# Kernel optimization log

Measured on AMD Instinct MI355X. Metric: run time of the kernel, lower is better.

The kernel has to match this reference:

```python
import jax, jax.numpy as jnp
import numpy as np

B, T, C, H, U = 16, 2048, 512, 4, 250
L, R = 1, 1              # l_order, r_order -> depthwise kernel size 3
K = L + R + 1
SMOOTH, NOISE = 1.0, 0.0  # smooth_factor, noise_threshold


def setup_inputs() -> dict:
    key = jax.random.key(0)
    k0, k1, k2, k3 = jax.random.split(key, 4)
    hidden = jax.random.normal(k0, (B, T, C), dtype=jnp.float32)
    mask = jnp.ones((B, 1, T), dtype=jnp.float32)
    target_label_length = jax.random.randint(k1, (B,), 0, U).astype(jnp.int32)
    # parameters
    conv_w = jax.random.normal(k2, (C, 1, K), dtype=jnp.float32) / np.sqrt(K)   # depthwise Conv1d weight [O, I/g=1, K]
    conv_b = jnp.zeros((C,), dtype=jnp.float32)
    lin_w = jax.random.normal(k3, (1, C), dtype=jnp.float32) / np.sqrt(C)       # cif_output Linear(idim, 1)
    lin_b = jnp.zeros((1,), dtype=jnp.float32)
    sigma = jnp.full((H,), 0.5, dtype=jnp.float32)
    sigma_bias = jnp.zeros((H,), dtype=jnp.float32)
    return {
        "hidden": hidden, "mask": mask, "target_label_length": target_label_length,
        "max_token": U, "conv_w": conv_w, "conv_b": conv_b,
        "lin_w": lin_w, "lin_b": lin_b, "sigma": sigma, "sigma_bias": sigma_bias,
    }


def reference(hidden, mask, target_label_length, max_token, conv_w, conv_b, lin_w, lin_b, sigma, sigma_bias):
    b, t, c = hidden.shape
    h = sigma.shape[0]
    # --- alpha prediction branch ---
    context = jnp.swapaxes(hidden, 1, 2)                       # [B, C, T]
    queries = jnp.pad(context, ((0, 0), (0, 0), (L, R)))       # ConstantPad1d((l, r), 0)
    memory = jax.lax.conv_general_dilated(
        queries, conv_w, window_strides=(1,), padding='VALID',
        feature_group_count=c, dimension_numbers=('NCH', 'OIH', 'NCH'))
    memory = memory + conv_b[None, :, None]
    out = jnp.swapaxes(memory + context, 1, 2)                 # [B, T, C]  (dropout = identity in eval)
    out = jax.nn.relu(out)
    out = out @ lin_w.T + lin_b                                # [B, T, 1]
    alphas = jax.nn.relu(jax.nn.sigmoid(out) * SMOOTH - NOISE)
    mask_bt1 = jnp.swapaxes(mask, -1, -2)                      # [B, T, 1]
    alphas = (alphas * mask_bt1)[..., 0]                       # [B, T]
    mask_bt = mask_bt1[..., 0]                                 # [B, T]
    # --- CIF scaling to target length ---
    target_length = target_label_length.astype(jnp.float32)   # [B]
    token_num = alphas.sum(-1)                                 # [B] (pre-scaling, as in torch)
    alphas = alphas * (target_length / token_num)[:, None]
    alignment = jnp.cumsum(alphas, axis=-1)                    # [B, T]
    # --- Gaussian soft-segment attention ---
    fire_positions = jnp.arange(max_token, dtype=alphas.dtype) + 0.5            # [U]
    dist = fire_positions[None, None, :, None] - alignment[:, None, None, :]    # [B, 1, U, T]
    scores = -(dist * sigma[None, :, None, None]) ** 2 + sigma_bias[None, :, None, None]  # [B, H, U, T]
    scores = jnp.where(mask_bt[:, None, None, :] > 0, scores, -jnp.inf)
    weights = jax.nn.softmax(scores, axis=-1)                  # [B, H, U, T]
    n_hidden = hidden.reshape(b, t, h, c // h).transpose(0, 2, 1, 3)            # [B, H, T, Dh]
    acoustic = jnp.einsum('bhut,bhtd->bhud', weights, n_hidden)                 # [B, H, U, Dh]
    acoustic_embeds = acoustic.transpose(0, 2, 1, 3).reshape(b, max_token, c)   # [B, U, C]
    return acoustic_embeds, token_num, alphas
```

## Files before the change

kernel.cpp:

```cpp
#include <hip/hip_runtime.h>
#include <hip/hip_bf16.h>

namespace {
constexpr int kB = 16, kT = 2048, kC = 512, kH = 4, kU = 250, kDH = 128;
constexpr int kDS = 4;
constexpr int kDW = 32;
constexpr int kTT = 256;
constexpr int kNST = kT / kTT;
constexpr int kPitch = 264;
}

typedef __attribute__((ext_vector_type(8))) short short8;
typedef __attribute__((ext_vector_type(4))) float float4v;

__device__ __forceinline__ short f2bf(float x) {
    union { float f; unsigned int u; } v; v.f = x;
    unsigned int r = (v.u + 0x7FFFu + ((v.u >> 16) & 1u)) >> 16;
    return (short)r;
}

__global__ __launch_bounds__(256) void k1_alpha(
    const float* __restrict__ hid, const float* __restrict__ mask,
    const float* __restrict__ conv_w, const float* __restrict__ conv_b,
    const float* __restrict__ lin_w, const float* __restrict__ lin_b,
    float* __restrict__ alpha_raw)
{
    __shared__ float halo[4][2][512];
    const int wave = threadIdx.x >> 6, lane = threadIdx.x & 63;
    const int b = blockIdx.x >> 6;
    const int tblk = (blockIdx.x & 63) << 5;
    const int t0 = tblk + wave * 8;
    const int c0 = lane * 8;

    float cw[24], cb[8], lw[8];
    #pragma unroll
    for (int i = 0; i < 6; i++) *(float4*)&cw[i*4] = ((const float4*)(conv_w + c0*3))[i];
    *(float4*)&cb[0] = *(const float4*)(conv_b + c0);
    *(float4*)&cb[4] = *(const float4*)(conv_b + c0 + 4);
    *(float4*)&lw[0] = *(const float4*)(lin_w + c0);
    *(float4*)&lw[4] = *(const float4*)(lin_w + c0 + 4);
    const float lb = lin_b[0];

    float r[10][8];
    const float* base = hid + ((size_t)b * kT + t0) * kC + c0;
    #pragma unroll
    for (int i = 1; i <= 8; i++) {
        const float* p = base + (ptrdiff_t)(i - 1) * kC;
        *(float4*)&r[i][0] = *(const float4*)p;
        *(float4*)&r[i][4] = *(const float4*)(p + 4);
    }
    *(float4*)&halo[wave][0][c0]     = *(float4*)&r[1][0];
    *(float4*)&halo[wave][0][c0 + 4] = *(float4*)&r[1][4];
    *(float4*)&halo[wave][1][c0]     = *(float4*)&r[8][0];
    *(float4*)&halo[wave][1][c0 + 4] = *(float4*)&r[8][4];

    if (wave == 0) {
        if (tblk > 0) {
            const float* p = base - kC;
            *(float4*)&r[0][0] = *(const float4*)p;
            *(float4*)&r[0][4] = *(const float4*)(p + 4);
        } else {
            #pragma unroll
            for (int j = 0; j < 8; j++) r[0][j] = 0.f;
        }
    }
    if (wave == 3) {
        if (tblk + 32 < kT) {
            const float* p = base + 8 * kC;
            *(float4*)&r[9][0] = *(const float4*)p;
            *(float4*)&r[9][4] = *(const float4*)(p + 4);
        } else {
            #pragma unroll
            for (int j = 0; j < 8; j++) r[9][j] = 0.f;
        }
    }
    __syncthreads();
    if (wave > 0) {
        *(float4*)&r[0][0] = *(float4*)&halo[wave - 1][1][c0];
        *(float4*)&r[0][4] = *(float4*)&halo[wave - 1][1][c0 + 4];
    }
    if (wave < 3) {
        *(float4*)&r[9][0] = *(float4*)&halo[wave + 1][0][c0];
        *(float4*)&r[9][4] = *(float4*)&halo[wave + 1][0][c0 + 4];
    }

    float sums[8];
    #pragma unroll
    for (int j = 0; j < 8; j++) {
        float acc = 0.f;
        #pragma unroll
        for (int k = 0; k < 8; k++) {
            float m = fmaf(r[j][k], cw[k*3],
                      fmaf(r[j+1][k], cw[k*3+1],
                      fmaf(r[j+2][k], cw[k*3+2], cb[k])));
            float v = m + r[j+1][k];
            v = v > 0.f ? v : 0.f;
            acc = fmaf(v, lw[k], acc);
        }
        #pragma unroll
        for (int off = 32; off >= 1; off >>= 1) acc += __shfl_xor(acc, off, 64);
        sums[j] = acc;
    }
    if (lane == 0) {
        #pragma unroll
        for (int j = 0; j < 8; j++) {
            float s = sums[j] + lb;
            float a = 1.f / (1.f + expf(-s));
            alpha_raw[(size_t)b * kT + t0 + j] = a * mask[(size_t)b * kT + t0 + j];
        }
    }
}

__global__ __launch_bounds__(1024) void k3_attn(
    const float* __restrict__ hid, const float* __restrict__ alpha_raw,
    const float* __restrict__ mask, const int* __restrict__ target,
    const float* __restrict__ sigma,
    float* __restrict__ out_ac, float* __restrict__ out_tok, float* __restrict__ out_alpha)
{
    __shared__ float al_s[kT];
    __shared__ unsigned short bT[2][kDW * kPitch];
    __shared__ float woff[16];
    __shared__ float s_tot;

    const int ds = blockIdx.x, h = blockIdx.y, b = blockIdx.z;
    const int tid = threadIdx.x;
    const int wave = tid >> 6, lane = tid & 63;
    const int lm = lane & 15, quad = lane >> 4;
    const float sig = sigma[h];

    const int dl = tid & 7;
    const int p  = tid >> 3;
    const float* hrow = hid + (size_t)b * kT * kC + h * kDH + ds * kDW + dl * 4;

    float4 a0, a1;
    {
        const float* src = hrow + (size_t)(2 * p) * kC;
        a0 = *(const float4*)src;
        a1 = *(const float4*)(src + kC);
    }

    float2 av = ((const float2*)(alpha_raw + (size_t)b * kT))[tid];
    float2 mv = ((const float2*)(mask + (size_t)b * kT))[tid];
    const float p0 = av.x, p1 = av.x + av.y;
    const float s = p1;
    float sc = s;
    #pragma unroll
    for (int off = 1; off <= 32; off <<= 1) {
        float v = __shfl_up(sc, off, 64);
        sc = (lane >= off) ? sc + v : sc;
    }
    if (lane == 63) woff[wave] = sc;
    __syncthreads();
    if (tid == 0) {
        float run = 0.f;
        #pragma unroll
        for (int w = 0; w < 16; w++) { float x = woff[w]; woff[w] = run; run += x; }
        s_tot = run;
    }
    __syncthreads();
    const float tot = s_tot;
    const float scale = (tot != 0.f) ? ((float)target[b] / tot) : 0.f;
    const float basev = woff[wave] + (sc - s);
    {
        float c0 = (basev + p0) * scale;
        float c1 = (basev + p1) * scale;
        float2 alv;
        alv.x = (mv.x > 0.f) ? c0 : 1.0e30f;
        alv.y = (mv.y > 0.f) ? c1 : 1.0e30f;
        ((float2*)al_s)[tid] = alv;
    }
    if (ds == 0 && h == 0) {
        if (tid == 0) out_tok[b] = tot;
        float2 oa; oa.x = av.x * scale; oa.y = av.y * scale;
        ((float2*)(out_alpha + (size_t)b * kT))[tid] = oa;
    }
    __syncthreads();

    const int u_base = wave * 16;
    const float du = (float)(u_base + lm) + 0.5f;
    const float dusig = du * sig;
    int pos = 0;
    #pragma unroll
    for (int stp = 1024; stp >= 1; stp >>= 1) {
        int np = pos + stp;
        pos = (al_s[np - 1] < du) ? np : pos;
    }
    float d1 = (pos < kT) ? al_s[pos] - du : 3.0e30f;
    float d0 = (pos > 0) ? du - al_s[pos - 1] : 3.0e30f;
    float dmin = fminf(d0, d1);
    float ms = fminf(dmin, 1.0e4f) * sig;
    const float mu_pos = ms * ms;

    float dmax_l = fminf(dmin, 1.0e4f);
    #pragma unroll
    for (int off = 8; off >= 1; off >>= 1) dmax_l = fmaxf(dmax_l, __shfl_xor(dmax_l, off, 64));
    const float c21 = (sig > 1e-3f) ? 21.0f / (sig * sig) : 9.0e60f;
    const float bound = sqrtf(fmaf(dmax_l, dmax_l, c21));
    const float lo_b = (float)u_base + 0.5f - bound;
    const float hi_b = (float)u_base + 15.5f + bound;
    int p_lo = 0, p_hi = 0;
    #pragma unroll
    for (int stp = 1024; stp >= 1; stp >>= 1) {
        int n1 = p_lo + stp; p_lo = (al_s[n1 - 1] < lo_b) ? n1 : p_lo;
        int n2 = p_hi + stp; p_hi = (al_s[n2 - 1] < hi_b) ? n2 : p_hi;
    }
    const int ks_lo = p_lo >> 5;
    const int ks_end = (p_hi + 31) >> 5;

    float4v acc0 = (float4v)(0.f), acc1 = (float4v)(0.f);
    float lsum = 0.f;

    int buf = 0;
    for (int st = 0; st < kNST; st++) {
        {
            const float* q0 = (const float*)&a0;
            const float* q1 = (const float*)&a1;
            #pragma unroll
            for (int e = 0; e < 4; e++) {
                unsigned int lo = (unsigned int)(unsigned short)f2bf(q0[e]);
                unsigned int hi = (unsigned int)(unsigned short)f2bf(q1[e]);
                *(unsigned int*)&bT[buf][(dl * 4 + e) * kPitch + 2 * p] = lo | (hi << 16);
            }
        }
        __syncthreads();
        if (st + 1 < kNST) {
            const float* src = hrow + (size_t)((st + 1) * kTT + 2 * p) * kC;
            a0 = *(const float4*)src;
            a1 = *(const float4*)(src + kC);
        }

        #pragma unroll
        for (int ks = 0; ks < 8; ks++) {
            const int kg = st * 8 + ks;
            if (kg < ks_lo || kg >= ks_end) continue;
            const int kb = kg * 32;

            float alv[8];
            *(float4*)&alv[0] = *(const float4*)&al_s[kb + quad * 8];
            *(float4*)&alv[4] = *(const float4*)&al_s[kb + quad * 8 + 4];

            short8 afrag;
            #pragma unroll
            for (int j = 0; j < 8; j++) {
                float d = fmaf(-alv[j], sig, dusig);
                float e = __expf(fmaf(-d, d, mu_pos));
                lsum += e;
                afrag[j] = f2bf(e);
            }
            short8 bf0 = *(const short8*)&bT[buf][lm * kPitch + ks * 32 + quad * 8];
            short8 bf1 = *(const short8*)&bT[buf][(16 + lm) * kPitch + ks * 32 + quad * 8];
            acc0 = __builtin_amdgcn_mfma_f32_16x16x32_bf16(afrag, bf0, acc0, 0, 0, 0);
            acc1 = __builtin_amdgcn_mfma_f32_16x16x32_bf16(afrag, bf1, acc1, 0, 0, 0);
        }
        buf ^= 1;
    }

    float lv = lsum;
    lv += __shfl_xor(lv, 16, 64);
    lv += __shfl_xor(lv, 32, 64);
    #pragma unroll
    for (int r = 0; r < 4; r++) {
        const int ur = quad * 4 + r;
        float rl = __shfl(lv, ur, 64);
        float linv = (rl > 1e-30f) ? 1.f / rl : 0.f;
        const int u = u_base + ur;
        if (u < kU) {
            float* dst = out_ac + ((size_t)(b * kU + u)) * kC + h * kDH + ds * kDW + lm;
            dst[0]  = acc0[r] * linv;
            dst[16] = acc1[r] * linv;
        }
    }
}

extern "C" void kernel_launch(void* const* d_in, const int* in_sizes, int n_in,
                              void* d_out, int out_size, void* d_ws, size_t ws_size,
                              hipStream_t stream) {
    const float* hid    = (const float*)d_in[0];
    const float* mask   = (const float*)d_in[1];
    const int*   tgt    = (const int*)d_in[2];
    const float* conv_w = (const float*)d_in[4];
    const float* conv_b = (const float*)d_in[5];
    const float* lin_w  = (const float*)d_in[6];
    const float* lin_b  = (const float*)d_in[7];
    const float* sigma  = (const float*)d_in[8];

    float* alpha_raw = (float*)d_ws;

    float* out_ac    = (float*)d_out;
    float* out_tok   = out_ac + (size_t)kB * kU * kC;
    float* out_alpha = out_tok + kB;

    k1_alpha<<<kB * kT / 32, 256, 0, stream>>>(hid, mask, conv_w, conv_b, lin_w, lin_b, alpha_raw);
    k3_attn<<<dim3(kDS, kH, kB), 1024, 0, stream>>>(hid, alpha_raw, mask, tgt, sigma,
                                                    out_ac, out_tok, out_alpha);
}
```

Baseline: 131.3 us.

## Fuse alpha prediction into attention kernel with grid-wide barrier and full-T LDS staging

Merges the alpha-prediction kernel into the attention kernel. Each block computes partial conv/linear logits for its 32-channel slice while staging all of T as bf16 in LDS, then accumulates them into a global buffer with atomics. A spin-wait grid barrier on a global counter follows, after which the attention loop runs only over the relevant T range from the resident LDS copy. This removes one launch and the double-buffered streaming pass, but adds a memset, float atomics whose order is nondeterministic, and a barrier that deadlocks (or bails out via the guard) if the 256 blocks are not all co-resident.

```diff
diff --git a/kernel.cpp b/kernel.cpp
--- a/kernel.cpp
+++ b/kernel.cpp
@@ -1,5 +1,4 @@
 #include <hip/hip_runtime.h>
-#include <hip/hip_bf16.h>
 
 namespace {
 constexpr int kB = 16, kT = 2048, kC = 512, kH = 4, kU = 250, kDH = 128;
@@ -7,7 +6,8 @@
 constexpr int kDW = 32;
 constexpr int kTT = 256;
 constexpr int kNST = kT / kTT;
-constexpr int kPitch = 264;
+constexpr int kPitch = 2056;
+constexpr int kNB = kDS * kH * kB;
 }
 
 typedef __attribute__((ext_vector_type(8))) short short8;
@@ -19,131 +19,156 @@
     return (short)r;
 }
 
-__global__ __launch_bounds__(256) void k1_alpha(
+__global__ __launch_bounds__(1024) void fused_pif(
     const float* __restrict__ hid, const float* __restrict__ mask,
+    const int* __restrict__ target, const float* __restrict__ sigma,
     const float* __restrict__ conv_w, const float* __restrict__ conv_b,
     const float* __restrict__ lin_w, const float* __restrict__ lin_b,
-    float* __restrict__ alpha_raw)
-{
-    __shared__ float halo[4][2][512];
-    const int wave = threadIdx.x >> 6, lane = threadIdx.x & 63;
-    const int b = blockIdx.x >> 6;
-    const int tblk = (blockIdx.x & 63) << 5;
-    const int t0 = tblk + wave * 8;
-    const int c0 = lane * 8;
-
-    float cw[24], cb[8], lw[8];
-    #pragma unroll
-    for (int i = 0; i < 6; i++) *(float4*)&cw[i*4] = ((const float4*)(conv_w + c0*3))[i];
-    *(float4*)&cb[0] = *(const float4*)(conv_b + c0);
-    *(float4*)&cb[4] = *(const float4*)(conv_b + c0 + 4);
-    *(float4*)&lw[0] = *(const float4*)(lin_w + c0);
-    *(float4*)&lw[4] = *(const float4*)(lin_w + c0 + 4);
-    const float lb = lin_b[0];
-
-    float r[10][8];
-    const float* base = hid + ((size_t)b * kT + t0) * kC + c0;
-    #pragma unroll
-    for (int i = 1; i <= 8; i++) {
-        const float* p = base + (ptrdiff_t)(i - 1) * kC;
-        *(float4*)&r[i][0] = *(const float4*)p;
-        *(float4*)&r[i][4] = *(const float4*)(p + 4);
-    }
-    *(float4*)&halo[wave][0][c0]     = *(float4*)&r[1][0];
-    *(float4*)&halo[wave][0][c0 + 4] = *(float4*)&r[1][4];
-    *(float4*)&halo[wave][1][c0]     = *(float4*)&r[8][0];
-    *(float4*)&halo[wave][1][c0 + 4] = *(float4*)&r[8][4];
-
-    if (wave == 0) {
-        if (tblk > 0) {
-            const float* p = base - kC;
-            *(float4*)&r[0][0] = *(const float4*)p;
-            *(float4*)&r[0][4] = *(const float4*)(p + 4);
-        } else {
-            #pragma unroll
-            for (int j = 0; j < 8; j++) r[0][j] = 0.f;
-        }
-    }
-    if (wave == 3) {
-        if (tblk + 32 < kT) {
-            const float* p = base + 8 * kC;
-            *(float4*)&r[9][0] = *(const float4*)p;
-            *(float4*)&r[9][4] = *(const float4*)(p + 4);
-        } else {
-            #pragma unroll
-            for (int j = 0; j < 8; j++) r[9][j] = 0.f;
-        }
-    }
-    __syncthreads();
-    if (wave > 0) {
-        *(float4*)&r[0][0] = *(float4*)&halo[wave - 1][1][c0];
-        *(float4*)&r[0][4] = *(float4*)&halo[wave - 1][1][c0 + 4];
-    }
-    if (wave < 3) {
-        *(float4*)&r[9][0] = *(float4*)&halo[wave + 1][0][c0];
-        *(float4*)&r[9][4] = *(float4*)&halo[wave + 1][0][c0 + 4];
-    }
-
-    float sums[8];
-    #pragma unroll
-    for (int j = 0; j < 8; j++) {
-        float acc = 0.f;
-        #pragma unroll
-        for (int k = 0; k < 8; k++) {
-            float m = fmaf(r[j][k], cw[k*3],
-                      fmaf(r[j+1][k], cw[k*3+1],
-                      fmaf(r[j+2][k], cw[k*3+2], cb[k])));
-            float v = m + r[j+1][k];
-            v = v > 0.f ? v : 0.f;
-            acc = fmaf(v, lw[k], acc);
-        }
-        #pragma unroll
-        for (int off = 32; off >= 1; off >>= 1) acc += __shfl_xor(acc, off, 64);
-        sums[j] = acc;
-    }
-    if (lane == 0) {
-        #pragma unroll
-        for (int j = 0; j < 8; j++) {
-            float s = sums[j] + lb;
-            float a = 1.f / (1.f + expf(-s));
-            alpha_raw[(size_t)b * kT + t0 + j] = a * mask[(size_t)b * kT + t0 + j];
-        }
-    }
-}
-
-__global__ __launch_bounds__(1024) void k3_attn(
-    const float* __restrict__ hid, const float* __restrict__ alpha_raw,
-    const float* __restrict__ mask, const int* __restrict__ target,
-    const float* __restrict__ sigma,
+    float* __restrict__ alpha_acc, unsigned int* __restrict__ counter,
     float* __restrict__ out_ac, float* __restrict__ out_tok, float* __restrict__ out_alpha)
 {
+    __shared__ unsigned short bV[kDW * kPitch];
     __shared__ float al_s[kT];
-    __shared__ unsigned short bT[2][kDW * kPitch];
+    __shared__ float wedge[16][8][8];
+    __shared__ float tedge[2][8][8];
     __shared__ float woff[16];
     __shared__ float s_tot;
 
     const int ds = blockIdx.x, h = blockIdx.y, b = blockIdx.z;
     const int tid = threadIdx.x;
     const int wave = tid >> 6, lane = tid & 63;
+    const int dl = tid & 7;
+    const int p  = tid >> 3;
+    const int pl = lane >> 3;
+    const int cbase = h * kDH + ds * kDW;
+    const int c0g = cbase + dl * 4;
+
+    float cw0[4], cw1[4], cw2[4], cb4[4], lw4[4];
+    {
+        float4 w0 = *(const float4*)(conv_w + c0g * 3);
+        float4 w1 = *(const float4*)(conv_w + c0g * 3 + 4);
+        float4 w2 = *(const float4*)(conv_w + c0g * 3 + 8);
+        cw0[0] = w0.x; cw1[0] = w0.y; cw2[0] = w0.z;
+        cw0[1] = w0.w; cw1[1] = w1.x; cw2[1] = w1.y;
+        cw0[2] = w1.z; cw1[2] = w1.w; cw2[2] = w2.x;
+        cw0[3] = w2.y; cw1[3] = w2.z; cw2[3] = w2.w;
+        *(float4*)cb4 = *(const float4*)(conv_b + c0g);
+        *(float4*)lw4 = *(const float4*)(lin_w + c0g);
+    }
+    float* acc_g = alpha_acc + (size_t)b * kT;
+    const float* hrow = hid + (size_t)b * kT * kC + c0g;
+
+    float4 a0, a1;
+    {
+        const float* s = hrow + (size_t)(2 * p) * kC;
+        a0 = *(const float4*)s;
+        a1 = *(const float4*)(s + kC);
+    }
+    for (int st = 0; st < kNST; st++) {
+        #pragma unroll
+        for (int e = 0; e < 4; e++) {
+            unsigned int lo = (unsigned int)(unsigned short)f2bf(((const float*)&a0)[e]);
+            unsigned int hi = (unsigned int)(unsigned short)f2bf(((const float*)&a1)[e]);
+            *(unsigned int*)&bV[(dl * 4 + e) * kPitch + st * kTT + 2 * p] = lo | (hi << 16);
+        }
+        if (pl == 7) {
+            *(float4*)&wedge[wave][dl][0] = a0;
+            *(float4*)&wedge[wave][dl][4] = a1;
+            if (wave == 15) {
+                *(float4*)&tedge[st & 1][dl][0] = a0;
+                *(float4*)&tedge[st & 1][dl][4] = a1;
+            }
+        }
+        float4 n0 = a0, n1 = a1;
+        if (st + 1 < kNST) {
+            const float* s = hrow + (size_t)((st + 1) * kTT + 2 * p) * kC;
+            n0 = *(const float4*)s;
+            n1 = *(const float4*)(s + kC);
+        }
+        __syncthreads();
+
+        float pm2[4], pm1[4];
+        #pragma unroll
+        for (int e = 0; e < 4; e++) {
+            pm2[e] = __shfl_up(((const float*)&a0)[e], 8, 64);
+            pm1[e] = __shfl_up(((const float*)&a1)[e], 8, 64);
+        }
+        if (pl == 0) {
+            if (wave > 0) {
+                *(float4*)pm2 = *(const float4*)&wedge[wave - 1][dl][0];
+                *(float4*)pm1 = *(const float4*)&wedge[wave - 1][dl][4];
+            } else if (st > 0) {
+                *(float4*)pm2 = *(const float4*)&tedge[(st - 1) & 1][dl][0];
+                *(float4*)pm1 = *(const float4*)&tedge[(st - 1) & 1][dl][4];
+            } else {
+                pm2[0] = pm2[1] = pm2[2] = pm2[3] = 0.f;
+                pm1[0] = pm1[1] = pm1[2] = pm1[3] = 0.f;
+            }
+        }
+        float s_m1 = 0.f, s_0 = 0.f;
+        #pragma unroll
+        for (int e = 0; e < 4; e++) {
+            float x_m2 = pm2[e], x_m1 = pm1[e];
+            float x0 = ((const float*)&a0)[e], x1 = ((const float*)&a1)[e];
+            float m_a = fmaf(cw0[e], x_m2, fmaf(cw1[e], x_m1, fmaf(cw2[e], x0, cb4[e])));
+            float v_a = m_a + x_m1; v_a = v_a > 0.f ? v_a : 0.f;
+            s_m1 = fmaf(v_a, lw4[e], s_m1);
+            float m_b = fmaf(cw0[e], x_m1, fmaf(cw1[e], x0, fmaf(cw2[e], x1, cb4[e])));
+            float v_b = m_b + x0; v_b = v_b > 0.f ? v_b : 0.f;
+            s_0 = fmaf(v_b, lw4[e], s_0);
+        }
+        #pragma unroll
+        for (int off = 1; off <= 4; off <<= 1) {
+            s_m1 += __shfl_xor(s_m1, off, 64);
+            s_0  += __shfl_xor(s_0, off, 64);
+        }
+        if (dl == 0) {
+            const int t0 = st * kTT + 2 * p;
+            if (t0 > 0) atomicAdd(acc_g + (t0 - 1), s_m1);
+            atomicAdd(acc_g + t0, s_0);
+        }
+        __syncthreads();
+        a0 = n0; a1 = n1;
+    }
+    if (tid < 8) {
+        float sacc = 0.f;
+        #pragma unroll
+        for (int e = 0; e < 4; e++) {
+            float xm1 = tedge[1][dl][e];
+            float x0  = tedge[1][dl][4 + e];
+            float m = fmaf(cw0[e], xm1, fmaf(cw1[e], x0, cb4[e]));
+            float v = m + x0; v = v > 0.f ? v : 0.f;
+            sacc = fmaf(v, lw4[e], sacc);
+        }
+        #pragma unroll
+        for (int off = 1; off <= 4; off <<= 1) sacc += __shfl_xor(sacc, off, 64);
+        if (dl == 0) atomicAdd(acc_g + (kT - 1), sacc);
+    }
+
+    __threadfence();
+    __syncthreads();
+    if (tid == 0) {
+        __hip_atomic_fetch_add(counter, 1u, __ATOMIC_RELEASE, __HIP_MEMORY_SCOPE_AGENT);
+        long long guard = 0;
+        while (__hip_atomic_load(counter, __ATOMIC_ACQUIRE, __HIP_MEMORY_SCOPE_AGENT) < (unsigned)kNB) {
+            __builtin_amdgcn_s_sleep(2);
+            if (++guard > (3LL << 20)) break;
+        }
+    }
+    __syncthreads();
+
     const int lm = lane & 15, quad = lane >> 4;
     const float sig = sigma[h];
-
-    const int dl = tid & 7;
-    const int p  = tid >> 3;
-    const float* hrow = hid + (size_t)b * kT * kC + h * kDH + ds * kDW + dl * 4;
-
-    float4 a0, a1;
-    {
-        const float* src = hrow + (size_t)(2 * p) * kC;
-        a0 = *(const float4*)src;
-        a1 = *(const float4*)(src + kC);
-    }
-
-    float2 av = ((const float2*)(alpha_raw + (size_t)b * kT))[tid];
+    const float lb = lin_b[0];
+
+    float l0 = __hip_atomic_load(acc_g + 2 * tid,     __ATOMIC_RELAXED, __HIP_MEMORY_SCOPE_AGENT);
+    float l1 = __hip_atomic_load(acc_g + 2 * tid + 1, __ATOMIC_RELAXED, __HIP_MEMORY_SCOPE_AGENT);
     float2 mv = ((const float2*)(mask + (size_t)b * kT))[tid];
-    const float p0 = av.x, p1 = av.x + av.y;
-    const float s = p1;
-    float sc = s;
+    float aw0 = (1.f / (1.f + expf(-(l0 + lb)))) * mv.x;
+    float aw1 = (1.f / (1.f + expf(-(l1 + lb)))) * mv.y;
+
+    const float p0 = aw0, p1v = aw0 + aw1;
+    float sc = p1v;
     #pragma unroll
     for (int off = 1; off <= 32; off <<= 1) {
         float v = __shfl_up(sc, off, 64);
@@ -160,10 +185,10 @@
     __syncthreads();
     const float tot = s_tot;
     const float scale = (tot != 0.f) ? ((float)target[b] / tot) : 0.f;
-    const float basev = woff[wave] + (sc - s);
+    const float basev = woff[wave] + (sc - p1v);
     {
         float c0 = (basev + p0) * scale;
-        float c1 = (basev + p1) * scale;
+        float c1 = (basev + p1v) * scale;
         float2 alv;
         alv.x = (mv.x > 0.f) ? c0 : 1.0e30f;
         alv.y = (mv.y > 0.f) ? c1 : 1.0e30f;
@@ -171,7 +196,7 @@
     }
     if (ds == 0 && h == 0) {
         if (tid == 0) out_tok[b] = tot;
-        float2 oa; oa.x = av.x * scale; oa.y = av.y * scale;
+        float2 oa; oa.x = aw0 * scale; oa.y = aw1 * scale;
         ((float2*)(out_alpha + (size_t)b * kT))[tid] = oa;
     }
     __syncthreads();
@@ -210,49 +235,24 @@
     float4v acc0 = (float4v)(0.f), acc1 = (float4v)(0.f);
     float lsum = 0.f;
 
-    int buf = 0;
-    for (int st = 0; st < kNST; st++) {
-        {
-            const float* q0 = (const float*)&a0;
-            const float* q1 = (const float*)&a1;
-            #pragma unroll
-            for (int e = 0; e < 4; e++) {
-                unsigned int lo = (unsigned int)(unsigned short)f2bf(q0[e]);
-                unsigned int hi = (unsigned int)(unsigned short)f2bf(q1[e]);
-                *(unsigned int*)&bT[buf][(dl * 4 + e) * kPitch + 2 * p] = lo | (hi << 16);
-            }
-        }
-        __syncthreads();
-        if (st + 1 < kNST) {
-            const float* src = hrow + (size_t)((st + 1) * kTT + 2 * p) * kC;
-            a0 = *(const float4*)src;
-            a1 = *(const float4*)(src + kC);
-        }
-
-        #pragma unroll
-        for (int ks = 0; ks < 8; ks++) {
-            const int kg = st * 8 + ks;
-            if (kg < ks_lo || kg >= ks_end) continue;
-            const int kb = kg * 32;
-
-            float alv[8];
-            *(float4*)&alv[0] = *(const float4*)&al_s[kb + quad * 8];
-            *(float4*)&alv[4] = *(const float4*)&al_s[kb + quad * 8 + 4];
-
-            short8 afrag;
-            #pragma unroll
-            for (int j = 0; j < 8; j++) {
-                float d = fmaf(-alv[j], sig, dusig);
-                float e = __expf(fmaf(-d, d, mu_pos));
-                lsum += e;
-                afrag[j] = f2bf(e);
-            }
-            short8 bf0 = *(const short8*)&bT[buf][lm * kPitch + ks * 32 + quad * 8];
-            short8 bf1 = *(const short8*)&bT[buf][(16 + lm) * kPitch + ks * 32 + quad * 8];
-            acc0 = __builtin_amdgcn_mfma_f32_16x16x32_bf16(afrag, bf0, acc0, 0, 0, 0);
-            acc1 = __builtin_amdgcn_mfma_f32_16x16x32_bf16(afrag, bf1, acc1, 0, 0, 0);
-        }
-        buf ^= 1;
+    for (int kg = ks_lo; kg < ks_end; kg++) {
+        const int kb = kg * 32;
+        float alv[8];
+        *(float4*)&alv[0] = *(const float4*)&al_s[kb + quad * 8];
+        *(float4*)&alv[4] = *(const float4*)&al_s[kb + quad * 8 + 4];
+
+        short8 afrag;
+        #pragma unroll
+        for (int j = 0; j < 8; j++) {
+            float d = fmaf(-alv[j], sig, dusig);
+            float e = __expf(fmaf(-d, d, mu_pos));
+            lsum += e;
+            afrag[j] = f2bf(e);
+        }
+        short8 bf0 = *(const short8*)&bV[lm * kPitch + kb + quad * 8];
+        short8 bf1 = *(const short8*)&bV[(16 + lm) * kPitch + kb + quad * 8];
+        acc0 = __builtin_amdgcn_mfma_f32_16x16x32_bf16(afrag, bf0, acc0, 0, 0, 0);
+        acc1 = __builtin_amdgcn_mfma_f32_16x16x32_bf16(afrag, bf1, acc1, 0, 0, 0);
     }
 
     float lv = lsum;
@@ -284,13 +284,15 @@
     const float* lin_b  = (const float*)d_in[7];
     const float* sigma  = (const float*)d_in[8];
 
-    float* alpha_raw = (float*)d_ws;
+    float* alpha_acc = (float*)d_ws;
+    unsigned int* counter = (unsigned int*)((char*)d_ws + (size_t)kB * kT * 4);
 
     float* out_ac    = (float*)d_out;
     float* out_tok   = out_ac + (size_t)kB * kU * kC;
     float* out_alpha = out_tok + kB;
 
-    k1_alpha<<<kB * kT / 32, 256, 0, stream>>>(hid, mask, conv_w, conv_b, lin_w, lin_b, alpha_raw);
-    k3_attn<<<dim3(kDS, kH, kB), 1024, 0, stream>>>(hid, alpha_raw, mask, tgt, sigma,
-                                                    out_ac, out_tok, out_alpha);
-}
+    hipMemsetAsync(d_ws, 0, (size_t)kB * kT * 4 + 64, stream);
+    fused_pif<<<dim3(kDS, kH, kB), 1024, 0, stream>>>(
+        hid, mask, tgt, sigma, conv_w, conv_b, lin_w, lin_b,
+        alpha_acc, counter, out_ac, out_tok, out_alpha);
+}
```

Measured after the change: 237.7 us. 1.81x slower.

## Emit transposed bf16 hidden in alpha kernel, split scan, window-only attention loop

Applied to the files above, without the earlier changes.

The alpha kernel now also writes a transposed bf16 copy of hidden (channel-major, padded pitch) to workspace using packed bf16 conversion. A separate small kernel does the cumsum, scaling and the token_num/alpha outputs. The attention kernel is regridded over (u-group, head, batch) with 256 threads, and reads MFMA B operands straight from global memory only over the Gaussian window, skipping the per-block LDS transpose of the full T range. exp is computed via v_exp_f32 with log2e folded into sigma. This trades an extra global write/read of a bf16 copy and an extra launch for removing redundant full-sequence loads and conversions in the attention kernel.

```diff
diff --git a/kernel.cpp b/kernel.cpp
--- a/kernel.cpp
+++ b/kernel.cpp
@@ -1,29 +1,29 @@
 #include <hip/hip_runtime.h>
-#include <hip/hip_bf16.h>
 
 namespace {
 constexpr int kB = 16, kT = 2048, kC = 512, kH = 4, kU = 250, kDH = 128;
-constexpr int kDS = 4;
-constexpr int kDW = 32;
-constexpr int kTT = 256;
-constexpr int kNST = kT / kTT;
-constexpr int kPitch = 264;
+constexpr int kPitchT = 2056;
 }
 
 typedef __attribute__((ext_vector_type(8))) short short8;
 typedef __attribute__((ext_vector_type(4))) float float4v;
 
-__device__ __forceinline__ short f2bf(float x) {
-    union { float f; unsigned int u; } v; v.f = x;
-    unsigned int r = (v.u + 0x7FFFu + ((v.u >> 16) & 1u)) >> 16;
-    return (short)r;
+__device__ __forceinline__ unsigned int pk_bf16(float lo, float hi) {
+    unsigned int r;
+    asm volatile("v_cvt_pk_bf16_f32 %0, %1, %2" : "=v"(r) : "v"(lo), "v"(hi));
+    return r;
+}
+__device__ __forceinline__ float exp2_fast(float x) {
+    float r;
+    asm volatile("v_exp_f32 %0, %1" : "=v"(r) : "v"(x));
+    return r;
 }
 
 __global__ __launch_bounds__(256) void k1_alpha(
     const float* __restrict__ hid, const float* __restrict__ mask,
     const float* __restrict__ conv_w, const float* __restrict__ conv_b,
     const float* __restrict__ lin_w, const float* __restrict__ lin_b,
-    float* __restrict__ alpha_raw)
+    float* __restrict__ alpha_raw, unsigned short* __restrict__ Vt)
 {
     __shared__ float halo[4][2][512];
     const int wave = threadIdx.x >> 6, lane = threadIdx.x & 63;
@@ -74,6 +74,17 @@
             for (int j = 0; j < 8; j++) r[9][j] = 0.f;
         }
     }
+
+    #pragma unroll
+    for (int e = 0; e < 8; e++) {
+        unsigned int vw[4];
+        vw[0] = pk_bf16(r[1][e], r[2][e]);
+        vw[1] = pk_bf16(r[3][e], r[4][e]);
+        vw[2] = pk_bf16(r[5][e], r[6][e]);
+        vw[3] = pk_bf16(r[7][e], r[8][e]);
+        *(uint4*)(Vt + ((size_t)b * kC + c0 + e) * kPitchT + t0) = *(const uint4*)vw;
+    }
+
     __syncthreads();
     if (wave > 0) {
         *(float4*)&r[0][0] = *(float4*)&halo[wave - 1][1][c0];
@@ -111,74 +122,86 @@
     }
 }
 
-__global__ __launch_bounds__(1024) void k3_attn(
-    const float* __restrict__ hid, const float* __restrict__ alpha_raw,
-    const float* __restrict__ mask, const int* __restrict__ target,
-    const float* __restrict__ sigma,
-    float* __restrict__ out_ac, float* __restrict__ out_tok, float* __restrict__ out_alpha)
+__global__ __launch_bounds__(256) void k2_scan(
+    const float* __restrict__ alpha_raw, const float* __restrict__ mask,
+    const int* __restrict__ target,
+    float* __restrict__ al, float* __restrict__ out_tok, float* __restrict__ out_alpha)
+{
+    __shared__ float woff[4];
+    __shared__ float s_tot;
+    const int b = blockIdx.x, tid = threadIdx.x;
+    const int wave = tid >> 6, lane = tid & 63;
+
+    float a[8], m[8];
+    const float* ar = alpha_raw + (size_t)b * kT + tid * 8;
+    const float* mr = mask + (size_t)b * kT + tid * 8;
+    *(float4*)&a[0] = *(const float4*)ar;
+    *(float4*)&a[4] = *(const float4*)(ar + 4);
+    *(float4*)&m[0] = *(const float4*)mr;
+    *(float4*)&m[4] = *(const float4*)(mr + 4);
+
+    float pre[8]; float run = 0.f;
+    #pragma unroll
+    for (int j = 0; j < 8; j++) { run += a[j]; pre[j] = run; }
+    float sc = run;
+    #pragma unroll
+    for (int off = 1; off <= 32; off <<= 1) {
+        float v = __shfl_up(sc, off, 64);
+        sc = (lane >= off) ? sc + v : sc;
+    }
+    if (lane == 63) woff[wave] = sc;
+    __syncthreads();
+    if (tid == 0) {
+        float r2 = 0.f;
+        #pragma unroll
+        for (int w = 0; w < 4; w++) { float x = woff[w]; woff[w] = r2; r2 += x; }
+        s_tot = r2;
+    }
+    __syncthreads();
+    const float tot = s_tot;
+    const float scale = (tot != 0.f) ? ((float)target[b] / tot) : 0.f;
+    const float basev = woff[wave] + (sc - run);
+
+    float alv[8], oav[8];
+    #pragma unroll
+    for (int j = 0; j < 8; j++) {
+        alv[j] = (m[j] > 0.f) ? (basev + pre[j]) * scale : 1.0e30f;
+        oav[j] = a[j] * scale;
+    }
+    float* alw = al + (size_t)b * kT + tid * 8;
+    float* oaw = out_alpha + (size_t)b * kT + tid * 8;
+    *(float4*)alw       = *(const float4*)&alv[0];
+    *(float4*)(alw + 4) = *(const float4*)&alv[4];
+    *(float4*)oaw       = *(const float4*)&oav[0];
+    *(float4*)(oaw + 4) = *(const float4*)&oav[4];
+    if (tid == 0) out_tok[b] = tot;
+}
+
+__global__ __launch_bounds__(256, 2) void k3_attn(
+    const unsigned short* __restrict__ Vt, const float* __restrict__ al,
+    const float* __restrict__ sigma, float* __restrict__ out_ac)
 {
     __shared__ float al_s[kT];
-    __shared__ unsigned short bT[2][kDW * kPitch];
-    __shared__ float woff[16];
-    __shared__ float s_tot;
-
-    const int ds = blockIdx.x, h = blockIdx.y, b = blockIdx.z;
+
+    const int ug = blockIdx.x, h = blockIdx.y, b = blockIdx.z;
     const int tid = threadIdx.x;
     const int wave = tid >> 6, lane = tid & 63;
     const int lm = lane & 15, quad = lane >> 4;
+    const int ut = wave & 1, dh = wave >> 1;
+    const int u0 = ug * 32 + ut * 16;
+    const int cb = h * kDH + dh * 64;
     const float sig = sigma[h];
-
-    const int dl = tid & 7;
-    const int p  = tid >> 3;
-    const float* hrow = hid + (size_t)b * kT * kC + h * kDH + ds * kDW + dl * 4;
-
-    float4 a0, a1;
+    const float sigL = sig * 1.2011224f;
+
     {
-        const float* src = hrow + (size_t)(2 * p) * kC;
-        a0 = *(const float4*)src;
-        a1 = *(const float4*)(src + kC);
-    }
-
-    float2 av = ((const float2*)(alpha_raw + (size_t)b * kT))[tid];
-    float2 mv = ((const float2*)(mask + (size_t)b * kT))[tid];
-    const float p0 = av.x, p1 = av.x + av.y;
-    const float s = p1;
-    float sc = s;
-    #pragma unroll
-    for (int off = 1; off <= 32; off <<= 1) {
-        float v = __shfl_up(sc, off, 64);
-        sc = (lane >= off) ? sc + v : sc;
-    }
-    if (lane == 63) woff[wave] = sc;
+        const float4* alg = (const float4*)(al + (size_t)b * kT);
+        ((float4*)al_s)[tid]       = alg[tid];
+        ((float4*)al_s)[tid + 256] = alg[tid + 256];
+    }
     __syncthreads();
-    if (tid == 0) {
-        float run = 0.f;
-        #pragma unroll
-        for (int w = 0; w < 16; w++) { float x = woff[w]; woff[w] = run; run += x; }
-        s_tot = run;
-    }
-    __syncthreads();
-    const float tot = s_tot;
-    const float scale = (tot != 0.f) ? ((float)target[b] / tot) : 0.f;
-    const float basev = woff[wave] + (sc - s);
-    {
-        float c0 = (basev + p0) * scale;
-        float c1 = (basev + p1) * scale;
-        float2 alv;
-        alv.x = (mv.x > 0.f) ? c0 : 1.0e30f;
-        alv.y = (mv.y > 0.f) ? c1 : 1.0e30f;
-        ((float2*)al_s)[tid] = alv;
-    }
-    if (ds == 0 && h == 0) {
-        if (tid == 0) out_tok[b] = tot;
-        float2 oa; oa.x = av.x * scale; oa.y = av.y * scale;
-        ((float2*)(out_alpha + (size_t)b * kT))[tid] = oa;
-    }
-    __syncthreads();
-
-    const int u_base = wave * 16;
-    const float du = (float)(u_base + lm) + 0.5f;
-    const float dusig = du * sig;
+
+    const float du = (float)(u0 + lm) + 0.5f;
+    const float duL = du * sigL;
     int pos = 0;
     #pragma unroll
     for (int stp = 1024; stp >= 1; stp >>= 1) {
@@ -188,7 +211,7 @@
     float d1 = (pos < kT) ? al_s[pos] - du : 3.0e30f;
     float d0 = (pos > 0) ? du - al_s[pos - 1] : 3.0e30f;
     float dmin = fminf(d0, d1);
-    float ms = fminf(dmin, 1.0e4f) * sig;
+    float ms = fminf(dmin, 1.0e4f) * sigL;
     const float mu_pos = ms * ms;
 
     float dmax_l = fminf(dmin, 1.0e4f);
@@ -196,8 +219,8 @@
     for (int off = 8; off >= 1; off >>= 1) dmax_l = fmaxf(dmax_l, __shfl_xor(dmax_l, off, 64));
     const float c21 = (sig > 1e-3f) ? 21.0f / (sig * sig) : 9.0e60f;
     const float bound = sqrtf(fmaf(dmax_l, dmax_l, c21));
-    const float lo_b = (float)u_base + 0.5f - bound;
-    const float hi_b = (float)u_base + 15.5f + bound;
+    const float lo_b = (float)u0 + 0.5f - bound;
+    const float hi_b = (float)u0 + 15.5f + bound;
     int p_lo = 0, p_hi = 0;
     #pragma unroll
     for (int stp = 1024; stp >= 1; stp >>= 1) {
@@ -208,51 +231,41 @@
     const int ks_end = (p_hi + 31) >> 5;
 
     float4v acc0 = (float4v)(0.f), acc1 = (float4v)(0.f);
+    float4v acc2 = (float4v)(0.f), acc3 = (float4v)(0.f);
     float lsum = 0.f;
 
-    int buf = 0;
-    for (int st = 0; st < kNST; st++) {
-        {
-            const float* q0 = (const float*)&a0;
-            const float* q1 = (const float*)&a1;
-            #pragma unroll
-            for (int e = 0; e < 4; e++) {
-                unsigned int lo = (unsigned int)(unsigned short)f2bf(q0[e]);
-                unsigned int hi = (unsigned int)(unsigned short)f2bf(q1[e]);
-                *(unsigned int*)&bT[buf][(dl * 4 + e) * kPitch + 2 * p] = lo | (hi << 16);
-            }
-        }
-        __syncthreads();
-        if (st + 1 < kNST) {
-            const float* src = hrow + (size_t)((st + 1) * kTT + 2 * p) * kC;
-            a0 = *(const float4*)src;
-            a1 = *(const float4*)(src + kC);
-        }
-
-        #pragma unroll
-        for (int ks = 0; ks < 8; ks++) {
-            const int kg = st * 8 + ks;
-            if (kg < ks_lo || kg >= ks_end) continue;
-            const int kb = kg * 32;
-
-            float alv[8];
-            *(float4*)&alv[0] = *(const float4*)&al_s[kb + quad * 8];
-            *(float4*)&alv[4] = *(const float4*)&al_s[kb + quad * 8 + 4];
-
-            short8 afrag;
-            #pragma unroll
-            for (int j = 0; j < 8; j++) {
-                float d = fmaf(-alv[j], sig, dusig);
-                float e = __expf(fmaf(-d, d, mu_pos));
-                lsum += e;
-                afrag[j] = f2bf(e);
-            }
-            short8 bf0 = *(const short8*)&bT[buf][lm * kPitch + ks * 32 + quad * 8];
-            short8 bf1 = *(const short8*)&bT[buf][(16 + lm) * kPitch + ks * 32 + quad * 8];
-            acc0 = __builtin_amdgcn_mfma_f32_16x16x32_bf16(afrag, bf0, acc0, 0, 0, 0);
-            acc1 = __builtin_amdgcn_mfma_f32_16x16x32_bf16(afrag, bf1, acc1, 0, 0, 0);
-        }
-        buf ^= 1;
+    const unsigned short* vrow = Vt + ((size_t)b * kC + cb + lm) * kPitchT + quad * 8;
+
+    #pragma unroll 2
+    for (int kg = ks_lo; kg < ks_end; kg++) {
+        const int kb = kg * 32;
+        float alv[8];
+        *(float4*)&alv[0] = *(const float4*)&al_s[kb + quad * 8];
+        *(float4*)&alv[4] = *(const float4*)&al_s[kb + quad * 8 + 4];
+
+        float ev[8];
+        #pragma unroll
+        for (int j = 0; j < 8; j++) {
+            float d = fmaf(-alv[j], sigL, duL);
+            float e = exp2_fast(fmaf(-d, d, mu_pos));
+            lsum += e;
+            ev[j] = e;
+        }
+        union { short8 s; unsigned int w[4]; } af;
+        af.w[0] = pk_bf16(ev[0], ev[1]);
+        af.w[1] = pk_bf16(ev[2], ev[3]);
+        af.w[2] = pk_bf16(ev[4], ev[5]);
+        af.w[3] = pk_bf16(ev[6], ev[7]);
+
+        const unsigned short* vp = vrow + kb;
+        short8 bf0 = *(const short8*)(vp);
+        short8 bf1 = *(const short8*)(vp + 16 * kPitchT);
+        short8 bf2 = *(const short8*)(vp + 32 * kPitchT);
+        short8 bf3 = *(const short8*)(vp + 48 * kPitchT);
+        acc0 = __builtin_amdgcn_mfma_f32_16x16x32_bf16(af.s, bf0, acc0, 0, 0, 0);
+        acc1 = __builtin_amdgcn_mfma_f32_16x16x32_bf16(af.s, bf1, acc1, 0, 0, 0);
+        acc2 = __builtin_amdgcn_mfma_f32_16x16x32_bf16(af.s, bf2, acc2, 0, 0, 0);
+        acc3 = __builtin_amdgcn_mfma_f32_16x16x32_bf16(af.s, bf3, acc3, 0, 0, 0);
     }
 
     float lv = lsum;
@@ -263,11 +276,13 @@
         const int ur = quad * 4 + r;
         float rl = __shfl(lv, ur, 64);
         float linv = (rl > 1e-30f) ? 1.f / rl : 0.f;
-        const int u = u_base + ur;
+        const int u = u0 + ur;
         if (u < kU) {
-            float* dst = out_ac + ((size_t)(b * kU + u)) * kC + h * kDH + ds * kDW + lm;
+            float* dst = out_ac + ((size_t)(b * kU + u)) * kC + cb + lm;
             dst[0]  = acc0[r] * linv;
             dst[16] = acc1[r] * linv;
+            dst[32] = acc2[r] * linv;
+            dst[48] = acc3[r] * linv;
         }
     }
 }
@@ -285,12 +300,15 @@
     const float* sigma  = (const float*)d_in[8];
 
     float* alpha_raw = (float*)d_ws;
+    float* al        = (float*)((char*)d_ws + 131072);
+    unsigned short* Vt = (unsigned short*)((char*)d_ws + 262144);
 
     float* out_ac    = (float*)d_out;
     float* out_tok   = out_ac + (size_t)kB * kU * kC;
     float* out_alpha = out_tok + kB;
 
-    k1_alpha<<<kB * kT / 32, 256, 0, stream>>>(hid, mask, conv_w, conv_b, lin_w, lin_b, alpha_raw);
-    k3_attn<<<dim3(kDS, kH, kB), 1024, 0, stream>>>(hid, alpha_raw, mask, tgt, sigma,
-                                                    out_ac, out_tok, out_alpha);
-}
+    k1_alpha<<<kB * kT / 32, 256, 0, stream>>>(hid, mask, conv_w, conv_b, lin_w, lin_b,
+                                               alpha_raw, Vt);
+    k2_scan<<<kB, 256, 0, stream>>>(alpha_raw, mask, tgt, al, out_tok, out_alpha);
+    k3_attn<<<dim3(8, kH, kB), 256, 0, stream>>>(Vt, al, sigma, out_ac);
+}
```

Result: slower. 176.1 us (+34.2%).
